# Kernel tuning notes

Measured on AMD Instinct MI355X. Metric: run time of the kernel, lower is better.

Reference implementation:

```python
import jax, jax.numpy as jnp
import numpy as np

B, T, C = 32, 512, 32
D, H, DFF, NL = 512, 8, 2048, 3
P, STRIDE, PAD = 16, 8, 8
N = (T - P) // STRIDE + 2  # 64 patches
E = D // H


def _sinusoidal_pe(n, d):
    pos = np.arange(n, dtype=np.float32)[:, None]
    div = np.exp(np.arange(0, d, 2, dtype=np.float32) * -(np.log(10000.0) / d))
    pe = np.zeros((n, d), np.float32)
    pe[:, 0::2] = np.sin(pos * div)
    pe[:, 1::2] = np.cos(pos * div)
    return jnp.asarray(pe)


def setup_inputs() -> dict:
    key = jax.random.key(0)
    ks = jax.random.split(key, 16)
    s = 0.02
    inp = {
        'x_enc': jax.random.normal(ks[0], (B, T, C), jnp.float32),
        'W_val': jax.random.normal(ks[1], (P, D), jnp.float32) * s,
        'Wq': jax.random.normal(ks[2], (NL, D, D), jnp.float32) * s,
        'bq': jnp.zeros((NL, D), jnp.float32),
        'Wk': jax.random.normal(ks[3], (NL, D, D), jnp.float32) * s,
        'bk': jnp.zeros((NL, D), jnp.float32),
        'Wv': jax.random.normal(ks[4], (NL, D, D), jnp.float32) * s,
        'bv': jnp.zeros((NL, D), jnp.float32),
        'Wo': jax.random.normal(ks[5], (NL, D, D), jnp.float32) * s,
        'bo': jnp.zeros((NL, D), jnp.float32),
        'Wc1': jax.random.normal(ks[6], (NL, D, DFF), jnp.float32) * s,
        'bc1': jnp.zeros((NL, DFF), jnp.float32),
        'Wc2': jax.random.normal(ks[7], (NL, DFF, D), jnp.float32) * s,
        'bc2': jnp.zeros((NL, D), jnp.float32),
        'ln1_g': jnp.ones((NL, D), jnp.float32),
        'ln1_b': jnp.zeros((NL, D), jnp.float32),
        'ln2_g': jnp.ones((NL, D), jnp.float32),
        'ln2_b': jnp.zeros((NL, D), jnp.float32),
        'bn_g': jnp.ones((D,), jnp.float32),
        'bn_b': jnp.zeros((D,), jnp.float32),
        'W_head': jax.random.normal(ks[8], (D * N, T), jnp.float32) * s,
        'b_head': jnp.zeros((T,), jnp.float32),
    }
    return inp


def _ln(x, g, b, eps=1e-5):
    m = x.mean(-1, keepdims=True)
    v = ((x - m) ** 2).mean(-1, keepdims=True)
    return (x - m) / jnp.sqrt(v + eps) * g + b


def reference(x_enc, W_val, Wq, bq, Wk, bk, Wv, bv, Wo, bo, Wc1, bc1, Wc2, bc2,
              ln1_g, ln1_b, ln2_g, ln2_b, bn_g, bn_b, W_head, b_head):
    pe = _sinusoidal_pe(N, D)
    # instance normalization over time (means detached, as in torch .detach())
    means = jax.lax.stop_gradient(x_enc.mean(axis=1, keepdims=True))
    x = x_enc - means
    stdev = jnp.sqrt(x.var(axis=1, keepdims=True) + 1e-5)  # [B,1,C]
    x = x / stdev
    x = x.transpose(0, 2, 1)  # [B, C, T]
    # replication pad right by PAD, then unfold into patches [B,C,N,P]
    x = jnp.concatenate([x, jnp.broadcast_to(x[..., -1:], x.shape[:-1] + (PAD,))], axis=-1)
    idx = jnp.arange(N)[:, None] * STRIDE + jnp.arange(P)[None, :]
    xp = x[..., idx]
    tok = xp.reshape(B * C, N, P) @ W_val + pe  # [B*C, N, D]

    scale = 1.0 / np.sqrt(E).astype(np.float32)
    for i in range(NL):
        q = (tok @ Wq[i] + bq[i]).reshape(-1, N, H, E)
        k = (tok @ Wk[i] + bk[i]).reshape(-1, N, H, E)
        v = (tok @ Wv[i] + bv[i]).reshape(-1, N, H, E)
        scores = jnp.einsum('blhe,bshe->bhls', q, k)
        A = jax.nn.softmax(scale * scores, axis=-1)
        V = jnp.einsum('bhls,bshd->blhd', A, v).reshape(-1, N, D)
        tok = tok + (V @ Wo[i] + bo[i])
        y = _ln(tok, ln1_g[i], ln1_b[i])
        y = jax.nn.gelu(y @ Wc1[i] + bc1[i], approximate=False) @ Wc2[i] + bc2[i]
        tok = _ln(tok + y, ln2_g[i], ln2_b[i])

    # BatchNorm1d over d_model channels (batch statistics, biased variance)
    m = tok.mean(axis=(0, 1))
    var = tok.var(axis=(0, 1))
    tok = (tok - m) / jnp.sqrt(var + 1e-5) * bn_g + bn_b

    enc = tok.reshape(B, C, N, D).transpose(0, 1, 3, 2).reshape(B, C, D * N)
    dec = enc @ W_head + b_head          # [B, C, T]
    dec = dec.transpose(0, 2, 1)          # [B, T, C]
    dec = dec * stdev[:, 0, :][:, None, :] + means[:, 0, :][:, None, :]
    return dec
```

## Files before the change

kernel.cpp:

```cpp
#include <hip/hip_runtime.h>
#include <math.h>

namespace {
constexpr int kB = 32, kT = 512, kC = 32, kD = 512, kDFF = 2048, kNL = 3;
constexpr int kP = 16, kStride = 8, kN = 64;
constexpr int kR = kB * kC;
constexpr int kM = kR * kN;
constexpr size_t kWbElems = (size_t)1536 * 512 + 512 * 512 + 2048 * 512 + 512 * 2048;
}

typedef unsigned short u16;
typedef __attribute__((ext_vector_type(8))) short short8;
typedef __attribute__((ext_vector_type(4))) float f32x4;

__device__ __forceinline__ float b2f(u16 u) {
    return __uint_as_float(((unsigned int)u) << 16);
}
__device__ __forceinline__ u16 f2b(float f) {
    unsigned int x = __float_as_uint(f);
    return (u16)((x + 0x7fffu + ((x >> 16) & 1u)) >> 16);
}

__device__ __forceinline__ void async_copy16(const u16* g, u16* l) {
    __builtin_amdgcn_global_load_lds(
        (const __attribute__((address_space(1))) unsigned int*)g,
        (__attribute__((address_space(3))) unsigned int*)l, 16, 0, 0);
}

__global__ void fill_kernel(float* __restrict__ p, float val, int n)
{
    int i = blockIdx.x * blockDim.x + threadIdx.x;
    if (i < n) p[i] = val;
}

__global__ __launch_bounds__(256) void instnorm_stats_kernel(
    const float* __restrict__ x, float* __restrict__ means, float* __restrict__ stdev)
{
    int b = blockIdx.x;
    int c = threadIdx.x & 31;
    int g = threadIdx.x >> 5;
    float s = 0.f, sq = 0.f;
    for (int t = g; t < kT; t += 8) {
        float v = x[(size_t)(b * kT + t) * kC + c];
        s += v; sq += v * v;
    }
    __shared__ float ss[8][32], ssq[8][32];
    ss[g][c] = s; ssq[g][c] = sq;
    __syncthreads();
    if (g == 0) {
        float S = 0.f, SQ = 0.f;
        for (int i = 0; i < 8; i++) { S += ss[i][c]; SQ += ssq[i][c]; }
        float m = S / kT;
        float var = SQ / kT - m * m;
        means[b * kC + c] = m;
        stdev[b * kC + c] = sqrtf(var + 1e-5f);
    }
}

__global__ __launch_bounds__(256) void patch_embed_kernel(
    const float* __restrict__ x, const float* __restrict__ Wval,
    const float* __restrict__ means, const float* __restrict__ stdev,
    u16* __restrict__ tok)
{
    int m = blockIdx.x;
    int r = m >> 6, n = m & 63;
    int b = r >> 5, c = r & 31;
    __shared__ float patch[kP];
    if (threadIdx.x < kP) {
        int t = n * kStride + threadIdx.x;
        if (t > kT - 1) t = kT - 1;
        patch[threadIdx.x] = (x[(size_t)(b * kT + t) * kC + c] - means[r]) / stdev[r];
    }
    __syncthreads();
    for (int d = threadIdx.x; d < kD; d += 256) {
        float acc = 0.f;
        #pragma unroll
        for (int p = 0; p < kP; p++) acc += patch[p] * Wval[p * kD + d];
        int j = d >> 1;
        float freq = expf(-(float)(2 * j) * (9.210340371976184f / (float)kD));
        float ang = (float)n * freq;
        float pe = (d & 1) ? cosf(ang) : sinf(ang);
        tok[(size_t)m * kD + d] = f2b(acc + pe);
    }
}

__global__ __launch_bounds__(256) void transpose_cvt_kernel(
    const float* __restrict__ in, u16* __restrict__ outp,
    int ldi, int ldo, int zin, int zout)
{
    __shared__ float tile[64][65];
    const float* ib = in + (size_t)blockIdx.z * zin;
    u16* ob = outp + (size_t)blockIdx.z * zout;
    int k0 = blockIdx.x * 64, n0 = blockIdx.y * 64;
    int tn = threadIdx.x & 63, tk0 = threadIdx.x >> 6;
    #pragma unroll
    for (int kk = tk0; kk < 64; kk += 4)
        tile[kk][tn] = ib[(size_t)(k0 + kk) * ldi + n0 + tn];
    __syncthreads();
    int wk = threadIdx.x & 63, wn0 = threadIdx.x >> 6;
    #pragma unroll
    for (int nn = wn0; nn < 64; nn += 4)
        ob[(size_t)(n0 + nn) * ldo + k0 + wk] = f2b(tile[wk][nn]);
}

template<int EPI>
__global__ __launch_bounds__(256) void mfma_gemm(
    const u16* __restrict__ A, const u16* __restrict__ B,
    const float* __restrict__ bias, const float* __restrict__ auxb1,
    const float* __restrict__ auxb2,
    u16* __restrict__ C0, u16* __restrict__ C1, u16* __restrict__ C2,
    float* __restrict__ fout, const float* __restrict__ stdev,
    int K, int lda, int ldb, int ldc)
{
    __shared__ alignas(16) u16 As[128 * 64];
    __shared__ alignas(16) u16 Bs[128 * 64];

    const int tid  = threadIdx.x;
    const int lane = tid & 63;
    const int wave = tid >> 6;
    const int wm   = wave >> 1;
    const int wn   = wave & 1;

    const int nwg  = gridDim.x * gridDim.y;
    const int orig = blockIdx.y * gridDim.x + blockIdx.x;
    const int qq = nwg >> 3, rr = nwg & 7;
    const int xcd = orig & 7, loc = orig >> 3;
    const int wg  = (xcd < rr) ? (xcd * (qq + 1) + loc)
                               : (rr * (qq + 1) + (xcd - rr) * qq + loc);
    const int row0 = (wg / gridDim.x) * 128;
    const int col0 = (wg % gridDim.x) * 128;
    const size_t zoff = (size_t)blockIdx.z * K;

    const int srow = tid >> 3;
    const int scol = (((tid & 7) ^ (srow & 7)) << 3);
    const u16* const Ag = A + (size_t)(row0 + srow) * lda + zoff + scol;
    const u16* const Bg = B + (size_t)(col0 + srow) * ldb + zoff + scol;
    u16* const AsW = As + (wave << 9);
    u16* const BsW = Bs + (wave << 9);

    const int fr = lane & 15;
    const int pc = (lane >> 4) ^ (lane & 7);
    const int a0 = ((wm << 6) + fr) * 64 + (pc << 3);
    const int a1 = ((wm << 6) + fr) * 64 + ((pc ^ 4) << 3);
    const int b0 = ((wn << 6) + fr) * 64 + (pc << 3);
    const int b1 = ((wn << 6) + fr) * 64 + ((pc ^ 4) << 3);

    short8 af[4], bfr[4];
    f32x4 acc[4][4];
    #pragma unroll
    for (int i = 0; i < 4; i++)
        #pragma unroll
        for (int j = 0; j < 4; j++)
            acc[i][j] = (f32x4){0.f, 0.f, 0.f, 0.f};

    for (int kb = 0; kb < K; kb += 64) {
        __syncthreads();
        #pragma unroll
        for (int c = 0; c < 4; c++) {
            async_copy16(Ag + kb + (size_t)(c * 32) * lda, AsW + c * 2048);
            async_copy16(Bg + kb + (size_t)(c * 32) * ldb, BsW + c * 2048);
        }
        __syncthreads();
        #pragma unroll
        for (int mi = 0; mi < 4; mi++) af[mi]  = *(const short8*)&As[a0 + (mi << 10)];
        #pragma unroll
        for (int ni = 0; ni < 4; ni++) bfr[ni] = *(const short8*)&Bs[b0 + (ni << 10)];
        #pragma unroll
        for (int mi = 0; mi < 4; mi++)
            #pragma unroll
            for (int ni = 0; ni < 4; ni++)
                acc[mi][ni] = __builtin_amdgcn_mfma_f32_16x16x32_bf16(
                    af[mi], bfr[ni], acc[mi][ni], 0, 0, 0);
        #pragma unroll
        for (int mi = 0; mi < 4; mi++) af[mi]  = *(const short8*)&As[a1 + (mi << 10)];
        #pragma unroll
        for (int ni = 0; ni < 4; ni++) bfr[ni] = *(const short8*)&Bs[b1 + (ni << 10)];
        #pragma unroll
        for (int mi = 0; mi < 4; mi++)
            #pragma unroll
            for (int ni = 0; ni < 4; ni++)
                acc[mi][ni] = __builtin_amdgcn_mfma_f32_16x16x32_bf16(
                    af[mi], bfr[ni], acc[mi][ni], 0, 0, 0);
    }

    const int er = (lane >> 4) << 2;
    const int ec = lane & 15;
    u16* dsel = C0;
    const float* bsel = bias;
    if (EPI == 0) {
        int sub = col0 >> 9;
        dsel = (sub == 0) ? C0 : ((sub == 1) ? C1 : C2);
        bsel = (sub == 0) ? bias : ((sub == 1) ? auxb1 : auxb2);
    }
    #pragma unroll
    for (int mi = 0; mi < 4; mi++) {
        #pragma unroll
        for (int ni = 0; ni < 4; ni++) {
            #pragma unroll
            for (int i = 0; i < 4; i++) {
                int r  = row0 + (wm << 6) + (mi << 4) + er + i;
                int cc = col0 + (wn << 6) + (ni << 4) + ec;
                float v = acc[mi][ni][i];
                if (EPI == 0) {
                    int cl = cc & 511;
                    dsel[(size_t)r * 512 + cl] = f2b(v + bsel[cl]);
                } else if (EPI == 1) {
                    size_t o = (size_t)r * ldc + cc;
                    float bb2 = bias ? bias[cc] : 0.f;
                    C0[o] = f2b(b2f(C0[o]) + v + bb2);
                } else if (EPI == 2) {
                    size_t o = (size_t)r * ldc + cc;
                    float z = v + bias[cc];
                    C0[o] = f2b(0.5f * z * (1.f + erff(z * 0.7071067811865475f)));
                } else {
                    float vv = v * stdev[r];
                    atomicAdd(&fout[(((size_t)(r >> 5) * kT + cc) << 5) + (r & 31)], vv);
                }
            }
        }
    }
}

__global__ __launch_bounds__(256) void attn_mfma_kernel(
    u16* __restrict__ qbuf, const u16* __restrict__ kbuf,
    const u16* __restrict__ vbuf)
{
    __shared__ u16 P[4][64 * 64];
    const int tid = threadIdx.x;
    const int wave = tid >> 6, lane = tid & 63;
    const int quad = lane >> 4, l15 = lane & 15;
    const size_t base = (size_t)blockIdx.x * 64 * kD;
    u16* Pw = P[wave];

    for (int hh = 0; hh < 2; hh++) {
        const int h = wave * 2 + hh;
        const u16* qh = qbuf + base + h * 64;
        const u16* kh = kbuf + base + h * 64;
        const u16* vh = vbuf + base + h * 64;

        short8 af[4][2], bf[4][2];
        #pragma unroll
        for (int mi = 0; mi < 4; mi++)
            #pragma unroll
            for (int kt = 0; kt < 2; kt++)
                af[mi][kt] = *(const short8*)(qh + (size_t)(mi * 16 + l15) * kD
                                              + kt * 32 + quad * 8);
        #pragma unroll
        for (int ni = 0; ni < 4; ni++)
            #pragma unroll
            for (int kt = 0; kt < 2; kt++)
                bf[ni][kt] = *(const short8*)(kh + (size_t)(ni * 16 + l15) * kD
                                              + kt * 32 + quad * 8);
        f32x4 S[4][4];
        #pragma unroll
        for (int mi = 0; mi < 4; mi++)
            #pragma unroll
            for (int ni = 0; ni < 4; ni++)
                S[mi][ni] = (f32x4){0.f, 0.f, 0.f, 0.f};
        #pragma unroll
        for (int mi = 0; mi < 4; mi++)
            #pragma unroll
            for (int ni = 0; ni < 4; ni++) {
                S[mi][ni] = __builtin_amdgcn_mfma_f32_16x16x32_bf16(
                    af[mi][0], bf[ni][0], S[mi][ni], 0, 0, 0);
                S[mi][ni] = __builtin_amdgcn_mfma_f32_16x16x32_bf16(
                    af[mi][1], bf[ni][1], S[mi][ni], 0, 0, 0);
            }

        #pragma unroll
        for (int mi = 0; mi < 4; mi++) {
            #pragma unroll
            for (int i = 0; i < 4; i++) {
                float mx = -1e30f;
                #pragma unroll
                for (int ni = 0; ni < 4; ni++) {
                    float v = S[mi][ni][i] * 0.125f;
                    S[mi][ni][i] = v;
                    mx = fmaxf(mx, v);
                }
                #pragma unroll
                for (int off = 1; off < 16; off <<= 1)
                    mx = fmaxf(mx, __shfl_xor(mx, off));
                float sum = 0.f;
                #pragma unroll
                for (int ni = 0; ni < 4; ni++) {
                    float e = expf(S[mi][ni][i] - mx);
                    S[mi][ni][i] = e;
                    sum += e;
                }
                #pragma unroll
                for (int off = 1; off < 16; off <<= 1)
                    sum += __shfl_xor(sum, off);
                float inv = 1.f / sum;
                #pragma unroll
                for (int ni = 0; ni < 4; ni++)
                    Pw[(mi * 16 + quad * 4 + i) * 64 + ni * 16 + l15] =
                        f2b(S[mi][ni][i] * inv);
            }
        }
        __syncthreads();

        short8 bv[4][2];
        #pragma unroll
        for (int ni = 0; ni < 4; ni++)
            #pragma unroll
            for (int kt = 0; kt < 2; kt++)
                #pragma unroll
                for (int j = 0; j < 8; j++)
                    bv[ni][kt][j] = (short)vh[(size_t)(kt * 32 + quad * 8 + j) * kD
                                              + ni * 16 + l15];
        short8 pa[4][2];
        #pragma unroll
        for (int mi = 0; mi < 4; mi++)
            #pragma unroll
            for (int kt = 0; kt < 2; kt++)
                pa[mi][kt] = *(const short8*)&Pw[(mi * 16 + l15) * 64
                                                 + kt * 32 + quad * 8];
        f32x4 O[4][4];
        #pragma unroll
        for (int mi = 0; mi < 4; mi++)
            #pragma unroll
            for (int ni = 0; ni < 4; ni++)
                O[mi][ni] = (f32x4){0.f, 0.f, 0.f, 0.f};
        #pragma unroll
        for (int mi = 0; mi < 4; mi++)
            #pragma unroll
            for (int ni = 0; ni < 4; ni++) {
                O[mi][ni] = __builtin_amdgcn_mfma_f32_16x16x32_bf16(
                    pa[mi][0], bv[ni][0], O[mi][ni], 0, 0, 0);
                O[mi][ni] = __builtin_amdgcn_mfma_f32_16x16x32_bf16(
                    pa[mi][1], bv[ni][1], O[mi][ni], 0, 0, 0);
            }
        u16* qo = qbuf + base + h * 64;
        #pragma unroll
        for (int mi = 0; mi < 4; mi++)
            #pragma unroll
            for (int ni = 0; ni < 4; ni++)
                #pragma unroll
                for (int i = 0; i < 4; i++)
                    qo[(size_t)(mi * 16 + quad * 4 + i) * kD + ni * 16 + l15] =
                        f2b(O[mi][ni][i]);
        __syncthreads();
    }
}

__global__ __launch_bounds__(256) void ln_kernel(
    const u16* __restrict__ x, const float* __restrict__ g,
    const float* __restrict__ bb, u16* __restrict__ y)
{
    size_t row = (size_t)blockIdx.x * 4 + (threadIdx.x >> 6);
    int lane = threadIdx.x & 63;
    float v[8];
    float s = 0.f;
    #pragma unroll
    for (int i = 0; i < 8; i++) {
        v[i] = b2f(x[row * kD + lane + i * 64]);
        s += v[i];
    }
    #pragma unroll
    for (int off = 32; off; off >>= 1) s += __shfl_xor(s, off);
    float mean = s * (1.f / kD);
    float sq = 0.f;
    #pragma unroll
    for (int i = 0; i < 8; i++) { float d = v[i] - mean; sq += d * d; }
    #pragma unroll
    for (int off = 32; off; off >>= 1) sq += __shfl_xor(sq, off);
    float inv = 1.f / sqrtf(sq * (1.f / kD) + 1e-5f);
    #pragma unroll
    for (int i = 0; i < 8; i++) {
        int d = lane + i * 64;
        y[row * kD + d] = f2b((v[i] - mean) * inv * g[d] + bb[d]);
    }
}

__global__ void zero_kernel(float* __restrict__ p, int n)
{
    int i = blockIdx.x * blockDim.x + threadIdx.x;
    if (i < n) p[i] = 0.f;
}

__global__ __launch_bounds__(512) void bn_stats_kernel(
    const u16* __restrict__ tok, float* __restrict__ sums, float* __restrict__ sumsq)
{
    int d = threadIdx.x;
    float s = 0.f, sq = 0.f;
    int row0 = blockIdx.x * 256;
    for (int row = row0; row < row0 + 256; row++) {
        float v = b2f(tok[(size_t)row * kD + d]);
        s += v; sq += v * v;
    }
    atomicAdd(&sums[d], s);
    atomicAdd(&sumsq[d], sq);
}

__global__ __launch_bounds__(512) void bn_final_kernel(
    const float* __restrict__ sums, const float* __restrict__ sumsq,
    const float* __restrict__ g, const float* __restrict__ bb,
    float* __restrict__ scale, float* __restrict__ shift)
{
    int d = threadIdx.x;
    float mean = sums[d] / (float)kM;
    float var = sumsq[d] / (float)kM - mean * mean;
    float sc = g[d] / sqrtf(var + 1e-5f);
    scale[d] = sc;
    shift[d] = bb[d] - mean * sc;
}

__global__ __launch_bounds__(256) void bn_apply_kernel(
    u16* __restrict__ tok, const float* __restrict__ scale,
    const float* __restrict__ shift)
{
    size_t i = (size_t)blockIdx.x * 256 + threadIdx.x;
    int d = (int)(i & 511);
    tok[i] = f2b(b2f(tok[i]) * scale[d] + shift[d]);
}

__global__ __launch_bounds__(256) void head_init_kernel(
    float* __restrict__ out, const float* __restrict__ b_head,
    const float* __restrict__ stdev, const float* __restrict__ means)
{
    int i = blockIdx.x * 256 + threadIdx.x;
    int c = i & 31, t = (i >> 5) & 511, b = i >> 14;
    int r = b * 32 + c;
    out[i] = b_head[t] * stdev[r] + means[r];
}

extern "C" void kernel_launch(void* const* d_in, const int* in_sizes, int n_in,
                              void* d_out, int out_size, void* d_ws, size_t ws_size,
                              hipStream_t stream)
{
    const float* x_enc  = (const float*)d_in[0];
    const float* W_val  = (const float*)d_in[1];
    const float* Wq     = (const float*)d_in[2];
    const float* bq     = (const float*)d_in[3];
    const float* Wk     = (const float*)d_in[4];
    const float* bk     = (const float*)d_in[5];
    const float* Wv     = (const float*)d_in[6];
    const float* bv     = (const float*)d_in[7];
    const float* Wo     = (const float*)d_in[8];
    const float* bo     = (const float*)d_in[9];
    const float* Wc1    = (const float*)d_in[10];
    const float* bc1    = (const float*)d_in[11];
    const float* Wc2    = (const float*)d_in[12];
    const float* bc2    = (const float*)d_in[13];
    const float* ln1_g  = (const float*)d_in[14];
    const float* ln1_b  = (const float*)d_in[15];
    const float* ln2_g  = (const float*)d_in[16];
    const float* ln2_b  = (const float*)d_in[17];
    const float* bn_g   = (const float*)d_in[18];
    const float* bn_b   = (const float*)d_in[19];
    const float* W_head = (const float*)d_in[20];
    const float* b_head = (const float*)d_in[21];
    float* out = (float*)d_out;

    const size_t tailBytes = (2 * kR + 4 * kD) * sizeof(float);
    const size_t headWb = (size_t)512 * 32768;
    int CH = 0; size_t unit = 0, region = 0;
    const int cands[4] = {1024, 512, 256, 128};
    for (int ci = 0; ci < 4; ci++) {
        size_t u = (size_t)cands[ci] * 64 * kD;
        size_t reg = 3 * u + kWbElems;
        if (reg < headWb) reg = headWb;
        size_t need = ((size_t)kM * kD + reg) * 2 + tailBytes;
        if (need <= ws_size) { CH = cands[ci]; unit = u; region = reg; break; }
    }
    if (CH == 0) {
        hipLaunchKernelGGL(fill_kernel, dim3((out_size + 255) / 256), dim3(256), 0,
                           stream, out, 1.0e6f, out_size);
        return;
    }
    const int nch = kR / CH;
    const int chRows = CH * 64;

    u16* tokb = (u16*)d_ws;
    u16* s0  = tokb + (size_t)kM * kD;
    u16* s1  = s0 + unit;
    u16* s2  = s1 + unit;
    u16* wbL = s2 + unit;
    u16* wbH = s0;
    u16* wQKV = wbL;
    u16* wO   = wQKV + (size_t)1536 * 512;
    u16* wC1  = wO + (size_t)512 * 512;
    u16* wC2  = wC1 + (size_t)2048 * 512;
    float* tail = (float*)(s0 + region);
    float* means    = tail;
    float* stdevp   = means + kR;
    float* bn_sums  = stdevp + kR;
    float* bn_sumsq = bn_sums + kD;
    float* bn_scale = bn_sumsq + kD;
    float* bn_shift = bn_scale + kD;

    hipLaunchKernelGGL(instnorm_stats_kernel, dim3(kB), dim3(256), 0, stream,
                       x_enc, means, stdevp);
    hipLaunchKernelGGL(patch_embed_kernel, dim3(kM), dim3(256), 0, stream,
                       x_enc, W_val, means, stdevp, tokb);

    const dim3 blk(256);
    const dim3 tr8(8, 8, 1);
    const int mt = chRows / 128;

    for (int i = 0; i < kNL; i++) {
        const float* Wq_i = Wq + (size_t)i * kD * kD;
        const float* Wk_i = Wk + (size_t)i * kD * kD;
        const float* Wv_i = Wv + (size_t)i * kD * kD;
        const float* Wo_i = Wo + (size_t)i * kD * kD;
        const float* Wc1_i = Wc1 + (size_t)i * kD * kDFF;
        const float* Wc2_i = Wc2 + (size_t)i * kDFF * kD;
        const float* bq_i = bq + i * kD, *bk_i = bk + i * kD, *bv_i = bv + i * kD;

        hipLaunchKernelGGL(transpose_cvt_kernel, tr8, blk, 0, stream,
                           Wq_i, wQKV, kD, kD, 0, 0);
        hipLaunchKernelGGL(transpose_cvt_kernel, tr8, blk, 0, stream,
                           Wk_i, wQKV + (size_t)512 * 512, kD, kD, 0, 0);
        hipLaunchKernelGGL(transpose_cvt_kernel, tr8, blk, 0, stream,
                           Wv_i, wQKV + (size_t)1024 * 512, kD, kD, 0, 0);
        hipLaunchKernelGGL(transpose_cvt_kernel, tr8, blk, 0, stream,
                           Wo_i, wO, kD, kD, 0, 0);
        hipLaunchKernelGGL(transpose_cvt_kernel, dim3(8, 32, 1), blk, 0, stream,
                           Wc1_i, wC1, kDFF, kD, 0, 0);
        hipLaunchKernelGGL(transpose_cvt_kernel, dim3(32, 8, 1), blk, 0, stream,
                           Wc2_i, wC2, kD, kDFF, 0, 0);

        for (int ch = 0; ch < nch; ch++) {
            u16* tokc = tokb + (size_t)ch * chRows * kD;
            hipLaunchKernelGGL((mfma_gemm<0>), dim3(12, mt, 1), blk, 0, stream,
                               tokc, wQKV, bq_i, bk_i, bv_i, s0, s1, s2,
                               nullptr, nullptr, kD, kD, kD, kD);
            hipLaunchKernelGGL(attn_mfma_kernel, dim3(CH), blk, 0, stream,
                               s0, s1, s2);
            hipLaunchKernelGGL((mfma_gemm<1>), dim3(4, mt, 1), blk, 0, stream,
                               s0, wO, bo + i * kD, nullptr, nullptr,
                               tokc, nullptr, nullptr, nullptr, nullptr,
                               kD, kD, kD, kD);
            hipLaunchKernelGGL(ln_kernel, dim3(chRows / 4), blk, 0, stream,
                               tokc, ln1_g + i * kD, ln1_b + i * kD, s0);
            for (int half = 0; half < 2; half++) {
                const u16* wc1h = wC1 + (size_t)half * 1024 * 512;
                const u16* wc2h = wC2 + (size_t)half * 1024;
                const float* bc1h = bc1 + (size_t)i * kDFF + half * 1024;
                hipLaunchKernelGGL((mfma_gemm<2>), dim3(8, mt, 1), blk, 0, stream,
                                   s0, wc1h, bc1h, nullptr, nullptr,
                                   s1, nullptr, nullptr, nullptr, nullptr,
                                   kD, kD, kD, 1024);
                hipLaunchKernelGGL((mfma_gemm<1>), dim3(4, mt, 1), blk, 0, stream,
                                   s1, wc2h, (half == 0) ? (bc2 + i * kD) : nullptr,
                                   nullptr, nullptr, tokc, nullptr, nullptr,
                                   nullptr, nullptr, 1024, 1024, kDFF, kD);
            }
            hipLaunchKernelGGL(ln_kernel, dim3(chRows / 4), blk, 0, stream,
                               tokc, ln2_g + i * kD, ln2_b + i * kD, tokc);
        }
    }

    hipLaunchKernelGGL(zero_kernel, dim3(1), dim3(1024), 0, stream, bn_sums, 2 * kD);
    hipLaunchKernelGGL(bn_stats_kernel, dim3(kM / 256), dim3(512), 0, stream,
                       tokb, bn_sums, bn_sumsq);
    hipLaunchKernelGGL(bn_final_kernel, dim3(1), dim3(512), 0, stream,
                       bn_sums, bn_sumsq, bn_g, bn_b, bn_scale, bn_shift);
    hipLaunchKernelGGL(bn_apply_kernel, dim3((int)((size_t)kM * kD / 256)), blk, 0,
                       stream, tokb, bn_scale, bn_shift);

    hipLaunchKernelGGL(transpose_cvt_kernel, dim3(8, 8, 64), blk, 0, stream,
                       W_head, wbH, 64 * 512, 32768, 512, 512);
    hipLaunchKernelGGL(head_init_kernel, dim3(out_size / 256), blk, 0, stream,
                       out, b_head, stdevp, means);
    hipLaunchKernelGGL((mfma_gemm<3>), dim3(4, 8, 8), blk, 0, stream,
                       tokb, wbH, nullptr, nullptr, nullptr,
                       nullptr, nullptr, nullptr, out, stdevp,
                       4096, 32768, 32768, kT);
}
```

Baseline: 3.480 ms.

## Transpose V for vector loads in attention; split-K head GEMM with reduction kernel

A new kernel transposes each 64x64 V head tile in place, so the attention kernel can load V fragments as 16-byte vectors instead of scalar strided gathers. The head GEMM's split-K goes from 8 to 16 slices, and each slice writes plain partial sums to a scratch buffer instead of atomically adding into the output. A reduction kernel then sums the partials and applies bias, stdev and mean. This trades an extra launch plus scratch traffic for removing uncoalesced V reads and atomic contention.

```diff
diff --git a/kernel.cpp b/kernel.cpp
--- a/kernel.cpp
+++ b/kernel.cpp
@@ -104,12 +104,12 @@
 }
 
 template<int EPI>
-__global__ __launch_bounds__(256) void mfma_gemm(
+__device__ __forceinline__ void gemm_body(
     const u16* __restrict__ A, const u16* __restrict__ B,
     const float* __restrict__ bias, const float* __restrict__ auxb1,
     const float* __restrict__ auxb2,
     u16* __restrict__ C0, u16* __restrict__ C1, u16* __restrict__ C2,
-    float* __restrict__ fout, const float* __restrict__ stdev,
+    float* __restrict__ fout,
     int K, int lda, int ldb, int ldc)
 {
     __shared__ alignas(16) u16 As[128 * 64];
@@ -213,11 +213,52 @@
                     float z = v + bias[cc];
                     C0[o] = f2b(0.5f * z * (1.f + erff(z * 0.7071067811865475f)));
                 } else {
-                    float vv = v * stdev[r];
-                    atomicAdd(&fout[(((size_t)(r >> 5) * kT + cc) << 5) + (r & 31)], vv);
+                    fout[((size_t)blockIdx.z << 19) + (size_t)r * ldc + cc] = v;
                 }
             }
         }
+    }
+}
+
+#define GEMM_ARGS \
+    const u16* __restrict__ A, const u16* __restrict__ B, \
+    const float* __restrict__ bias, const float* __restrict__ auxb1, \
+    const float* __restrict__ auxb2, \
+    u16* __restrict__ C0, u16* __restrict__ C1, u16* __restrict__ C2, \
+    float* __restrict__ fout, \
+    int K, int lda, int ldb, int ldc
+#define GEMM_PASS A, B, bias, auxb1, auxb2, C0, C1, C2, fout, K, lda, ldb, ldc
+
+__global__ __launch_bounds__(256) void gemm_qkv(GEMM_ARGS)   { gemm_body<0>(GEMM_PASS); }
+__global__ __launch_bounds__(256) void gemm_resid(GEMM_ARGS) { gemm_body<1>(GEMM_PASS); }
+__global__ __launch_bounds__(256) void gemm_gelu(GEMM_ARGS)  { gemm_body<2>(GEMM_PASS); }
+__global__ __launch_bounds__(256) void gemm_head(GEMM_ARGS)  { gemm_body<3>(GEMM_PASS); }
+
+__global__ __launch_bounds__(256) void vtr_kernel(u16* __restrict__ v)
+{
+    __shared__ u16 tl[4][64 * 72];
+    const int tid = threadIdx.x;
+    const int wave = tid >> 6, lane = tid & 63;
+    const int sr = lane >> 3, ch = lane & 7;
+    const int tile = blockIdx.x * 4 + wave;
+    const int series = tile >> 3, h = tile & 7;
+    u16* g = v + (size_t)series * 64 * kD + h * 64;
+    u16* T = tl[wave];
+    short8 rd[8];
+    #pragma unroll
+    for (int r = 0; r < 8; r++)
+        rd[r] = *(const short8*)(g + (size_t)(r * 8 + sr) * kD + ch * 8);
+    #pragma unroll
+    for (int r = 0; r < 8; r++)
+        *(short8*)&T[(r * 8 + sr) * 72 + ch * 8] = rd[r];
+    __syncthreads();
+    #pragma unroll
+    for (int r = 0; r < 8; r++) {
+        short8 wr;
+        #pragma unroll
+        for (int q = 0; q < 8; q++)
+            wr[q] = (short)T[(ch * 8 + q) * 72 + (r * 8 + sr)];
+        *(short8*)(g + (size_t)(r * 8 + sr) * kD + ch * 8) = wr;
     }
 }
 
@@ -305,10 +346,8 @@
         for (int ni = 0; ni < 4; ni++)
             #pragma unroll
             for (int kt = 0; kt < 2; kt++)
-                #pragma unroll
-                for (int j = 0; j < 8; j++)
-                    bv[ni][kt][j] = (short)vh[(size_t)(kt * 32 + quad * 8 + j) * kD
-                                              + ni * 16 + l15];
+                bv[ni][kt] = *(const short8*)(vh + (size_t)(ni * 16 + l15) * kD
+                                              + kt * 32 + quad * 8);
         short8 pa[4][2];
         #pragma unroll
         for (int mi = 0; mi < 4; mi++)
@@ -415,14 +454,18 @@
     tok[i] = f2b(b2f(tok[i]) * scale[d] + shift[d]);
 }
 
-__global__ __launch_bounds__(256) void head_init_kernel(
-    float* __restrict__ out, const float* __restrict__ b_head,
-    const float* __restrict__ stdev, const float* __restrict__ means)
-{
-    int i = blockIdx.x * 256 + threadIdx.x;
-    int c = i & 31, t = (i >> 5) & 511, b = i >> 14;
-    int r = b * 32 + c;
-    out[i] = b_head[t] * stdev[r] + means[r];
+__global__ __launch_bounds__(256) void head_reduce_kernel(
+    const float* __restrict__ part, const float* __restrict__ b_head,
+    const float* __restrict__ stdev, const float* __restrict__ means,
+    float* __restrict__ out)
+{
+    int j = blockIdx.x * 256 + threadIdx.x;
+    int r = j >> 9, t = j & 511;
+    float s = 0.f;
+    #pragma unroll
+    for (int z = 0; z < 16; z++) s += part[((size_t)z << 19) + j];
+    int b = r >> 5, c = r & 31;
+    out[(((size_t)b * kT + t) << 5) + c] = (s + b_head[t]) * stdev[r] + means[r];
 }
 
 extern "C" void kernel_launch(void* const* d_in, const int* in_sizes, int n_in,
@@ -523,14 +566,15 @@
 
         for (int ch = 0; ch < nch; ch++) {
             u16* tokc = tokb + (size_t)ch * chRows * kD;
-            hipLaunchKernelGGL((mfma_gemm<0>), dim3(12, mt, 1), blk, 0, stream,
+            hipLaunchKernelGGL(gemm_qkv, dim3(12, mt, 1), blk, 0, stream,
                                tokc, wQKV, bq_i, bk_i, bv_i, s0, s1, s2,
-                               nullptr, nullptr, kD, kD, kD, kD);
+                               nullptr, kD, kD, kD, kD);
+            hipLaunchKernelGGL(vtr_kernel, dim3(CH * 2), blk, 0, stream, s2);
             hipLaunchKernelGGL(attn_mfma_kernel, dim3(CH), blk, 0, stream,
                                s0, s1, s2);
-            hipLaunchKernelGGL((mfma_gemm<1>), dim3(4, mt, 1), blk, 0, stream,
+            hipLaunchKernelGGL(gemm_resid, dim3(4, mt, 1), blk, 0, stream,
                                s0, wO, bo + i * kD, nullptr, nullptr,
-                               tokc, nullptr, nullptr, nullptr, nullptr,
+                               tokc, nullptr, nullptr, nullptr,
                                kD, kD, kD, kD);
             hipLaunchKernelGGL(ln_kernel, dim3(chRows / 4), blk, 0, stream,
                                tokc, ln1_g + i * kD, ln1_b + i * kD, s0);
@@ -538,14 +582,14 @@
                 const u16* wc1h = wC1 + (size_t)half * 1024 * 512;
                 const u16* wc2h = wC2 + (size_t)half * 1024;
                 const float* bc1h = bc1 + (size_t)i * kDFF + half * 1024;
-                hipLaunchKernelGGL((mfma_gemm<2>), dim3(8, mt, 1), blk, 0, stream,
+                hipLaunchKernelGGL(gemm_gelu, dim3(8, mt, 1), blk, 0, stream,
                                    s0, wc1h, bc1h, nullptr, nullptr,
-                                   s1, nullptr, nullptr, nullptr, nullptr,
+                                   s1, nullptr, nullptr, nullptr,
                                    kD, kD, kD, 1024);
-                hipLaunchKernelGGL((mfma_gemm<1>), dim3(4, mt, 1), blk, 0, stream,
+                hipLaunchKernelGGL(gemm_resid, dim3(4, mt, 1), blk, 0, stream,
                                    s1, wc2h, (half == 0) ? (bc2 + i * kD) : nullptr,
                                    nullptr, nullptr, tokc, nullptr, nullptr,
-                                   nullptr, nullptr, 1024, 1024, kDFF, kD);
+                                   nullptr, 1024, 1024, kDFF, kD);
             }
             hipLaunchKernelGGL(ln_kernel, dim3(chRows / 4), blk, 0, stream,
                                tokc, ln2_g + i * kD, ln2_b + i * kD, tokc);
@@ -562,10 +606,10 @@
 
     hipLaunchKernelGGL(transpose_cvt_kernel, dim3(8, 8, 64), blk, 0, stream,
                        W_head, wbH, 64 * 512, 32768, 512, 512);
-    hipLaunchKernelGGL(head_init_kernel, dim3(out_size / 256), blk, 0, stream,
-                       out, b_head, stdevp, means);
-    hipLaunchKernelGGL((mfma_gemm<3>), dim3(4, 8, 8), blk, 0, stream,
+    hipLaunchKernelGGL(gemm_head, dim3(4, 8, 16), blk, 0, stream,
                        tokb, wbH, nullptr, nullptr, nullptr,
-                       nullptr, nullptr, nullptr, out, stdevp,
-                       4096, 32768, 32768, kT);
-}
+                       nullptr, nullptr, nullptr, (float*)s1,
+                       2048, 32768, 32768, kT);
+    hipLaunchKernelGGL(head_reduce_kernel, dim3(kR * kT / 256), blk, 0, stream,
+                       (const float*)s1, b_head, stdevp, means, out);
+}
```

Result: faster. 3.237 ms (-7.0%).
